# Kernel optimization log

Measured on AMD Instinct MI355X. Metric: run time of the kernel, lower is better.

## Reference

```python
import jax, jax.numpy as jnp
import numpy as np

N = 100000
E = 1600000
IN_C, HID_C, OUT_C, NUM_CLASSES = 128, 64, 64, 40


def glorot(key, shape):
    lim = float(np.sqrt(6.0 / (shape[0] + shape[1])))
    return jax.random.uniform(key, shape, jnp.float32, -lim, lim)


def setup_inputs() -> dict:
    key = jax.random.key(0)
    ks = jax.random.split(key, 8)
    x = jax.random.normal(ks[0], (N, IN_C), jnp.float32)
    edge_index = jax.random.randint(ks[1], (2, E), 0, N, jnp.int64)
    return {
        "x": x,
        "edge_index": edge_index,
        "W1": glorot(ks[2], (IN_C, HID_C)),
        "b1": jnp.zeros((HID_C,), jnp.float32),
        "W2": glorot(ks[3], (HID_C, OUT_C)),
        "b2": jnp.zeros((OUT_C,), jnp.float32),
        "Wf": glorot(ks[4], (OUT_C, NUM_CLASSES)),
        "bf": jnp.zeros((NUM_CLASSES,), jnp.float32),
    }


def gcn_conv(x, W, b, src, dst, n):
    # PyG GCNConv: out = D^{-1/2} (A + I) D^{-1/2} (x W) + b, self-loops added.
    h = x @ W  # [N, C_out]
    loop = jnp.arange(n, dtype=src.dtype)
    src_f = jnp.concatenate([src, loop])  # [E+N]
    dst_f = jnp.concatenate([dst, loop])
    deg = jax.ops.segment_sum(jnp.ones_like(dst_f, dtype=h.dtype), dst_f,
                              num_segments=n)  # in-degree incl. self-loop
    inv_sqrt = jnp.where(deg > 0, jax.lax.rsqrt(deg), 0.0)
    norm = inv_sqrt[src_f] * inv_sqrt[dst_f]  # [E+N]
    msg = h[src_f] * norm[:, None]  # gather + scale, [E+N, C_out]
    out = jax.ops.segment_sum(msg, dst_f, num_segments=n)  # scatter-add
    return out + b


def reference(x, edge_index, W1, b1, W2, b2, Wf, bf):
    src, dst = edge_index[0], edge_index[1]
    n = x.shape[0]
    h = jax.nn.relu(gcn_conv(x, W1, b1, src, dst, n))
    h = jax.nn.relu(gcn_conv(h, W2, b2, src, dst, n))
    return h @ Wf + bf
```

## Files before the change

### kernel.cpp

```cpp
#include <hip/hip_runtime.h>

constexpr int N_NODES = 100000;
constexpr int N_EDGES = 1600000;
constexpr int IN_C  = 128;
constexpr int HID_C = 64;
constexpr int NUM_CLASSES = 40;

constexpr int BSH = 9;
constexpr int BUCK_N = 1 << BSH;
constexpr int NBUCK = (N_NODES + BUCK_N - 1) >> BSH;
constexpr int BCAP = 9216;
constexpr int FS_EPT = 16;
constexpr int FS_T = 256;
constexpr int FS_CHUNK = FS_EPT * FS_T;
constexpr int FS_BLKS = (N_EDGES + FS_CHUNK - 1) / FS_CHUNK;

typedef __attribute__((ext_vector_type(8))) short bf16x8;
typedef __attribute__((ext_vector_type(4))) short short4v;
typedef __attribute__((ext_vector_type(4))) float f32x4;

__device__ __forceinline__ unsigned short f2bf(float f) {
    unsigned u = __float_as_uint(f);
    return (unsigned short)((u + 0x7FFFu + ((u >> 16) & 1u)) >> 16);
}
__device__ __forceinline__ float bf2f(unsigned short h) {
    return __uint_as_float((unsigned)h << 16);
}

__global__ void bucket_init_kernel(unsigned* __restrict__ gcur) {
    if (threadIdx.x < NBUCK) gcur[threadIdx.x] = 0u;
}

__global__ __launch_bounds__(FS_T) void fill_stage_kernel(
        const int* __restrict__ src, const int* __restrict__ dst,
        unsigned* __restrict__ gcur, unsigned* __restrict__ stage) {
    __shared__ unsigned hist[NBUCK];
    __shared__ unsigned rbase[NBUCK];
    int t = threadIdx.x;
    for (int i = t; i < NBUCK; i += FS_T) hist[i] = 0u;
    __syncthreads();
    int e0 = blockIdx.x * FS_CHUNK + t;
    unsigned pay[FS_EPT];
    unsigned br[FS_EPT];
#pragma unroll
    for (int i = 0; i < FS_EPT; ++i) {
        int e = e0 + i * FS_T;
        br[i] = 0xFFFFFFFFu; pay[i] = 0u;
        if (e < N_EDGES) {
            unsigned d = (unsigned)dst[e];
            unsigned s = (unsigned)src[e];
            unsigned b = d >> BSH;
            unsigned r = atomicAdd(&hist[b], 1u);
            pay[i] = (s << BSH) | (d & (BUCK_N - 1u));
            br[i]  = (b << 16) | r;
        }
    }
    __syncthreads();
    for (int i = t; i < NBUCK; i += FS_T) {
        unsigned c = hist[i];
        rbase[i] = c ? ((unsigned)i * BCAP + atomicAdd(&gcur[i], c)) : 0u;
    }
    __syncthreads();
#pragma unroll
    for (int i = 0; i < FS_EPT; ++i) {
        if (br[i] != 0xFFFFFFFFu) {
            unsigned bb = br[i] >> 16;
            unsigned idx = rbase[bb] + (br[i] & 0xFFFFu);
            if (idx < (bb + 1u) * BCAP) stage[idx] = pay[i];
        }
    }
}

__global__ __launch_bounds__(256) void scan_buckets_kernel(
        const unsigned* __restrict__ gcur, unsigned* __restrict__ bbase,
        unsigned* __restrict__ rowptr) {
    __shared__ unsigned s[256];
    int t = threadIdx.x;
    unsigned v = (t < NBUCK) ? gcur[t] : 0u;
    s[t] = v;
    __syncthreads();
    for (int off = 1; off < 256; off <<= 1) {
        unsigned u = (t >= off) ? s[t - off] : 0u;
        __syncthreads();
        s[t] += u;
        __syncthreads();
    }
    if (t < NBUCK) bbase[t] = s[t] - v;
    if (t == 255) rowptr[N_NODES] = s[255];
}

__global__ __launch_bounds__(512) void fill_final_kernel(
        const unsigned* __restrict__ gcur, const unsigned* __restrict__ bbase,
        const unsigned* __restrict__ stage, unsigned* __restrict__ rowptr,
        float* __restrict__ inv, unsigned* __restrict__ csr_src) {
    __shared__ unsigned cur[BUCK_N];
    __shared__ unsigned ps[512];
    __shared__ unsigned buf[BCAP];
    int b = blockIdx.x, t = threadIdx.x;
    int lo = b << BSH;
    int nn = min(BUCK_N, N_NODES - lo);
    unsigned c = min(gcur[b], (unsigned)BCAP);
    unsigned base = bbase[b];
    const unsigned* st = stage + (size_t)b * BCAP;
    cur[t] = 0u;
    __syncthreads();
    for (int i = t; i < (int)c; i += 512) atomicAdd(&cur[st[i] & (BUCK_N - 1u)], 1u);
    __syncthreads();
    unsigned d = cur[t];
    ps[t] = d;
    __syncthreads();
    for (int off = 1; off < 512; off <<= 1) {
        unsigned u = (t >= off) ? ps[t - off] : 0u;
        __syncthreads();
        ps[t] += u;
        __syncthreads();
    }
    unsigned off0 = ps[t] - d;
    if (t < nn) {
        rowptr[lo + t] = base + off0;
        inv[lo + t] = rsqrtf((float)(d + 1u));
    }
    __syncthreads();
    cur[t] = off0;
    __syncthreads();
    for (int i = t; i < (int)c; i += 512) {
        unsigned v = st[i];
        unsigned pos = atomicAdd(&cur[v & (BUCK_N - 1u)], 1u);
        buf[pos] = v >> BSH;
    }
    __syncthreads();
    for (int i = t; i < (int)c; i += 512) csr_src[base + i] = buf[i];
}

template <int K, bool BF>
__global__ __launch_bounds__(256) void gemm_mfma_kernel(
        const void* __restrict__ Xv, const float* __restrict__ W,
        const float* __restrict__ inv, unsigned short* __restrict__ out, int n) {
    __shared__ __align__(16) short Asd[64][K + 8];
    __shared__ __align__(16) short Bsd[64][K + 8];
    int t = threadIdx.x;
    int n0 = blockIdx.x * 64;
    if (BF) {
        const uint4* Xb = (const uint4*)Xv;
        for (int i = t; i < 64 * (K / 8); i += 256) {
            int row = i / (K / 8), seg = i % (K / 8);
            int node = n0 + row;
            uint4 v = {0, 0, 0, 0};
            if (node < n) v = Xb[(size_t)node * (K / 8) + seg];
            *(uint4*)&Asd[row][seg * 8] = v;
        }
    } else {
        const float* Xf = (const float*)Xv;
        for (int i = t; i < 64 * (K / 4); i += 256) {
            int row = i / (K / 4), seg = i % (K / 4);
            int node = n0 + row;
            float4 v = {0, 0, 0, 0};
            if (node < n) v = *(const float4*)&Xf[(size_t)node * K + seg * 4];
            short4v o;
            o.x = (short)f2bf(v.x); o.y = (short)f2bf(v.y);
            o.z = (short)f2bf(v.z); o.w = (short)f2bf(v.w);
            *(short4v*)&Asd[row][seg * 4] = o;
        }
    }
    for (int i = t; i < K * 16; i += 256) {
        int k = i >> 4, ng = i & 15;
        float4 v = *(const float4*)&W[(size_t)k * 64 + ng * 4];
        Bsd[ng * 4 + 0][k] = (short)f2bf(v.x);
        Bsd[ng * 4 + 1][k] = (short)f2bf(v.y);
        Bsd[ng * 4 + 2][k] = (short)f2bf(v.z);
        Bsd[ng * 4 + 3][k] = (short)f2bf(v.w);
    }
    __syncthreads();
    int wv = t >> 6, lane = t & 63;
    int m = lane & 15, quad = lane >> 4;
    int rowbase = wv * 16;
    f32x4 acc0 = {0,0,0,0}, acc1 = {0,0,0,0}, acc2 = {0,0,0,0}, acc3 = {0,0,0,0};
#pragma unroll
    for (int kb = 0; kb < K / 32; ++kb) {
        bf16x8 af = *(const bf16x8*)&Asd[rowbase + m][kb * 32 + quad * 8];
        bf16x8 b0 = *(const bf16x8*)&Bsd[ 0 + m][kb * 32 + quad * 8];
        bf16x8 b1 = *(const bf16x8*)&Bsd[16 + m][kb * 32 + quad * 8];
        bf16x8 b2 = *(const bf16x8*)&Bsd[32 + m][kb * 32 + quad * 8];
        bf16x8 b3 = *(const bf16x8*)&Bsd[48 + m][kb * 32 + quad * 8];
        acc0 = __builtin_amdgcn_mfma_f32_16x16x32_bf16(af, b0, acc0, 0, 0, 0);
        acc1 = __builtin_amdgcn_mfma_f32_16x16x32_bf16(af, b1, acc1, 0, 0, 0);
        acc2 = __builtin_amdgcn_mfma_f32_16x16x32_bf16(af, b2, acc2, 0, 0, 0);
        acc3 = __builtin_amdgcn_mfma_f32_16x16x32_bf16(af, b3, acc3, 0, 0, 0);
    }
    f32x4 accs[4] = {acc0, acc1, acc2, acc3};
#pragma unroll
    for (int r = 0; r < 4; ++r) {
        int node = n0 + rowbase + quad * 4 + r;
        if (node < n) {
            float sc = inv[node];
#pragma unroll
            for (int s = 0; s < 4; ++s)
                out[(size_t)node * 64 + s * 16 + m] = f2bf(accs[s][r] * sc);
        }
    }
}

__global__ __launch_bounds__(256) void agg_fused_kernel(
        const unsigned* __restrict__ rowptr, const unsigned* __restrict__ csr_src,
        const unsigned short* __restrict__ hs, const float* __restrict__ inv,
        const float* __restrict__ bias, unsigned short* __restrict__ out) {
    int node = blockIdx.x * 4 + (threadIdx.x >> 6);
    int lane = threadIdx.x & 63;
    int oct = lane >> 3;
    int cl  = lane & 7;
    unsigned beg = rowptr[node], end = rowptr[node + 1];
    float a0 = 0.f, a1 = 0.f, a2 = 0.f, a3 = 0.f;
    float a4 = 0.f, a5 = 0.f, a6 = 0.f, a7 = 0.f;
    const uint4* hsrow = (const uint4*)hs;
    for (unsigned base = beg; base < end; base += 64) {
        int navail = min((int)(end - base), 64);
        unsigned myidx = 0;
        if (lane < navail) myidx = csr_src[base + lane];
        int it8 = (navail + 7) & ~7;
        for (int i = oct; i < it8; i += 8) {
            unsigned s = __shfl(myidx, i);
            if (i < navail) {
                uint4 v = hsrow[(size_t)s * 8 + cl];
                a0 += __uint_as_float(v.x << 16);
                a1 += __uint_as_float(v.x & 0xFFFF0000u);
                a2 += __uint_as_float(v.y << 16);
                a3 += __uint_as_float(v.y & 0xFFFF0000u);
                a4 += __uint_as_float(v.z << 16);
                a5 += __uint_as_float(v.z & 0xFFFF0000u);
                a6 += __uint_as_float(v.w << 16);
                a7 += __uint_as_float(v.w & 0xFFFF0000u);
            }
        }
    }
    a0 += __shfl_xor(a0, 8);  a1 += __shfl_xor(a1, 8);
    a2 += __shfl_xor(a2, 8);  a3 += __shfl_xor(a3, 8);
    a4 += __shfl_xor(a4, 8);  a5 += __shfl_xor(a5, 8);
    a6 += __shfl_xor(a6, 8);  a7 += __shfl_xor(a7, 8);
    a0 += __shfl_xor(a0, 16); a1 += __shfl_xor(a1, 16);
    a2 += __shfl_xor(a2, 16); a3 += __shfl_xor(a3, 16);
    a4 += __shfl_xor(a4, 16); a5 += __shfl_xor(a5, 16);
    a6 += __shfl_xor(a6, 16); a7 += __shfl_xor(a7, 16);
    a0 += __shfl_xor(a0, 32); a1 += __shfl_xor(a1, 32);
    a2 += __shfl_xor(a2, 32); a3 += __shfl_xor(a3, 32);
    a4 += __shfl_xor(a4, 32); a5 += __shfl_xor(a5, 32);
    a6 += __shfl_xor(a6, 32); a7 += __shfl_xor(a7, 32);
    if (oct == 0) {
        uint4 sv = hsrow[(size_t)node * 8 + cl];
        float4 bv0 = *(const float4*)&bias[cl * 8];
        float4 bv1 = *(const float4*)&bias[cl * 8 + 4];
        float s = inv[node];
        float r0 = fmaxf(s * (a0 + __uint_as_float(sv.x << 16))        + bv0.x, 0.f);
        float r1 = fmaxf(s * (a1 + __uint_as_float(sv.x & 0xFFFF0000u)) + bv0.y, 0.f);
        float r2 = fmaxf(s * (a2 + __uint_as_float(sv.y << 16))        + bv0.z, 0.f);
        float r3 = fmaxf(s * (a3 + __uint_as_float(sv.y & 0xFFFF0000u)) + bv0.w, 0.f);
        float r4 = fmaxf(s * (a4 + __uint_as_float(sv.z << 16))        + bv1.x, 0.f);
        float r5 = fmaxf(s * (a5 + __uint_as_float(sv.z & 0xFFFF0000u)) + bv1.y, 0.f);
        float r6 = fmaxf(s * (a6 + __uint_as_float(sv.w << 16))        + bv1.z, 0.f);
        float r7 = fmaxf(s * (a7 + __uint_as_float(sv.w & 0xFFFF0000u)) + bv1.w, 0.f);
        uint4 o;
        o.x = (unsigned)f2bf(r0) | ((unsigned)f2bf(r1) << 16);
        o.y = (unsigned)f2bf(r2) | ((unsigned)f2bf(r3) << 16);
        o.z = (unsigned)f2bf(r4) | ((unsigned)f2bf(r5) << 16);
        o.w = (unsigned)f2bf(r6) | ((unsigned)f2bf(r7) << 16);
        ((uint4*)out)[(size_t)node * 8 + cl] = o;
    }
}

__global__ __launch_bounds__(320) void final_gemm_kernel(
        const unsigned short* __restrict__ H, const float* __restrict__ Wf,
        const float* __restrict__ bfv, float* __restrict__ out, int n) {
    constexpr int CK = 64, J = 40;
    __shared__ float Ws[CK * J];
    __shared__ float Hs[CK][132];
    int t = threadIdx.x;
    int n0 = blockIdx.x * 128;
    for (int i = t; i < CK * J / 4; i += 320)
        ((float4*)Ws)[i] = ((const float4*)Wf)[i];
    for (int i = t; i < 128 * 16; i += 320) {
        int row = i >> 4, kc = i & 15;
        int node = n0 + row;
        ushort4 v = {0, 0, 0, 0};
        if (node < n) v = *(const ushort4*)&H[(size_t)node * 64 + kc * 4];
        Hs[kc * 4 + 0][row] = bf2f(v.x);
        Hs[kc * 4 + 1][row] = bf2f(v.y);
        Hs[kc * 4 + 2][row] = bf2f(v.z);
        Hs[kc * 4 + 3][row] = bf2f(v.w);
    }
    __syncthreads();
    int cg = t % 10;
    int rg = t / 10;
    float4 a0 = {0,0,0,0}, a1 = {0,0,0,0}, a2 = {0,0,0,0}, a3 = {0,0,0,0};
#pragma unroll 8
    for (int k = 0; k < CK; ++k) {
        float4 b = *(const float4*)&Ws[k * J + cg * 4];
        float4 a = *(const float4*)&Hs[k][rg * 4];
        a0.x += a.x * b.x; a0.y += a.x * b.y; a0.z += a.x * b.z; a0.w += a.x * b.w;
        a1.x += a.y * b.x; a1.y += a.y * b.y; a1.z += a.y * b.z; a1.w += a.y * b.w;
        a2.x += a.z * b.x; a2.y += a.z * b.y; a2.z += a.z * b.z; a2.w += a.z * b.w;
        a3.x += a.w * b.x; a3.y += a.w * b.y; a3.z += a.w * b.z; a3.w += a.w * b.w;
    }
    float4 bv = *(const float4*)&bfv[cg * 4];
    float4 accs[4] = {a0, a1, a2, a3};
#pragma unroll
    for (int i = 0; i < 4; ++i) {
        int node = n0 + rg * 4 + i;
        if (node < n) {
            float4 r = accs[i];
            r.x += bv.x; r.y += bv.y; r.z += bv.z; r.w += bv.w;
            *(float4*)&out[(size_t)node * J + cg * 4] = r;
        }
    }
}

extern "C" void kernel_launch(void* const* d_in, const int* in_sizes, int n_in,
                              void* d_out, int out_size, void* d_ws, size_t ws_size,
                              hipStream_t stream) {
    const float* x  = (const float*)d_in[0];
    const int*   ei = (const int*)d_in[1];
    const float* W1 = (const float*)d_in[2];
    const float* b1 = (const float*)d_in[3];
    const float* W2 = (const float*)d_in[4];
    const float* b2 = (const float*)d_in[5];
    const float* Wf = (const float*)d_in[6];
    const float* bf = (const float*)d_in[7];
    float* out = (float*)d_out;

    const int* src = ei;
    const int* dst = ei + N_EDGES;

    char* ws = (char*)d_ws;
    unsigned* rowptr  = (unsigned*)(ws + 0);
    float*    inv     = (float*)   (ws + 400064);
    unsigned* gcur    = (unsigned*)(ws + 800064);
    unsigned* bbase   = (unsigned*)(ws + 800896);
    unsigned* csr_src = (unsigned*)(ws + 801792);
    unsigned short* A = (unsigned short*)(ws + 7201792);
    unsigned short* B = (unsigned short*)(ws + 20001792);
    unsigned* stage   = (unsigned*)A;

    bucket_init_kernel<<<1, 256, 0, stream>>>(gcur);
    fill_stage_kernel<<<FS_BLKS, FS_T, 0, stream>>>(src, dst, gcur, stage);
    scan_buckets_kernel<<<1, 256, 0, stream>>>(gcur, bbase, rowptr);
    fill_final_kernel<<<NBUCK, 512, 0, stream>>>(gcur, bbase, stage, rowptr, inv, csr_src);

    gemm_mfma_kernel<IN_C, false>
        <<<(N_NODES + 63) / 64, 256, 0, stream>>>(x, W1, inv, A, N_NODES);
    agg_fused_kernel<<<N_NODES / 4, 256, 0, stream>>>(rowptr, csr_src, A, inv, b1, B);

    gemm_mfma_kernel<HID_C, true>
        <<<(N_NODES + 63) / 64, 256, 0, stream>>>(B, W2, inv, A, N_NODES);
    agg_fused_kernel<<<N_NODES / 4, 256, 0, stream>>>(rowptr, csr_src, A, inv, b2, B);

    final_gemm_kernel<<<(N_NODES + 127) / 128, 320, 0, stream>>>(B, Wf, bf, out, N_NODES);
}
```

Before: 274.1 us.

## Map one node per 8-lane group in aggregation instead of one node per wave

The aggregation kernel now gives each wavefront 8 nodes, with one 8-lane group per node, so each group walks its own CSR row serially. Before, each wave served one node and split its edges across 8 octets. This removes the cross-octet shuffle reduction and the idle-lane waste on low-degree nodes (average degree is about 16). In exchange, the groups within a wave diverge when node degrees differ, and the per-edge index loads are no longer coalesced across the wave.

```diff
diff --git a/kernel.cpp b/kernel.cpp
--- a/kernel.cpp
+++ b/kernel.cpp
@@ -204,66 +204,46 @@
         const unsigned* __restrict__ rowptr, const unsigned* __restrict__ csr_src,
         const unsigned short* __restrict__ hs, const float* __restrict__ inv,
         const float* __restrict__ bias, unsigned short* __restrict__ out) {
-    int node = blockIdx.x * 4 + (threadIdx.x >> 6);
-    int lane = threadIdx.x & 63;
+    int t = threadIdx.x;
+    int lane = t & 63;
     int oct = lane >> 3;
     int cl  = lane & 7;
+    int node = blockIdx.x * 32 + (t >> 6) * 8 + oct;
     unsigned beg = rowptr[node], end = rowptr[node + 1];
     float a0 = 0.f, a1 = 0.f, a2 = 0.f, a3 = 0.f;
     float a4 = 0.f, a5 = 0.f, a6 = 0.f, a7 = 0.f;
     const uint4* hsrow = (const uint4*)hs;
-    for (unsigned base = beg; base < end; base += 64) {
-        int navail = min((int)(end - base), 64);
-        unsigned myidx = 0;
-        if (lane < navail) myidx = csr_src[base + lane];
-        int it8 = (navail + 7) & ~7;
-        for (int i = oct; i < it8; i += 8) {
-            unsigned s = __shfl(myidx, i);
-            if (i < navail) {
-                uint4 v = hsrow[(size_t)s * 8 + cl];
-                a0 += __uint_as_float(v.x << 16);
-                a1 += __uint_as_float(v.x & 0xFFFF0000u);
-                a2 += __uint_as_float(v.y << 16);
-                a3 += __uint_as_float(v.y & 0xFFFF0000u);
-                a4 += __uint_as_float(v.z << 16);
-                a5 += __uint_as_float(v.z & 0xFFFF0000u);
-                a6 += __uint_as_float(v.w << 16);
-                a7 += __uint_as_float(v.w & 0xFFFF0000u);
-            }
-        }
-    }
-    a0 += __shfl_xor(a0, 8);  a1 += __shfl_xor(a1, 8);
-    a2 += __shfl_xor(a2, 8);  a3 += __shfl_xor(a3, 8);
-    a4 += __shfl_xor(a4, 8);  a5 += __shfl_xor(a5, 8);
-    a6 += __shfl_xor(a6, 8);  a7 += __shfl_xor(a7, 8);
-    a0 += __shfl_xor(a0, 16); a1 += __shfl_xor(a1, 16);
-    a2 += __shfl_xor(a2, 16); a3 += __shfl_xor(a3, 16);
-    a4 += __shfl_xor(a4, 16); a5 += __shfl_xor(a5, 16);
-    a6 += __shfl_xor(a6, 16); a7 += __shfl_xor(a7, 16);
-    a0 += __shfl_xor(a0, 32); a1 += __shfl_xor(a1, 32);
-    a2 += __shfl_xor(a2, 32); a3 += __shfl_xor(a3, 32);
-    a4 += __shfl_xor(a4, 32); a5 += __shfl_xor(a5, 32);
-    a6 += __shfl_xor(a6, 32); a7 += __shfl_xor(a7, 32);
-    if (oct == 0) {
-        uint4 sv = hsrow[(size_t)node * 8 + cl];
-        float4 bv0 = *(const float4*)&bias[cl * 8];
-        float4 bv1 = *(const float4*)&bias[cl * 8 + 4];
-        float s = inv[node];
-        float r0 = fmaxf(s * (a0 + __uint_as_float(sv.x << 16))        + bv0.x, 0.f);
-        float r1 = fmaxf(s * (a1 + __uint_as_float(sv.x & 0xFFFF0000u)) + bv0.y, 0.f);
-        float r2 = fmaxf(s * (a2 + __uint_as_float(sv.y << 16))        + bv0.z, 0.f);
-        float r3 = fmaxf(s * (a3 + __uint_as_float(sv.y & 0xFFFF0000u)) + bv0.w, 0.f);
-        float r4 = fmaxf(s * (a4 + __uint_as_float(sv.z << 16))        + bv1.x, 0.f);
-        float r5 = fmaxf(s * (a5 + __uint_as_float(sv.z & 0xFFFF0000u)) + bv1.y, 0.f);
-        float r6 = fmaxf(s * (a6 + __uint_as_float(sv.w << 16))        + bv1.z, 0.f);
-        float r7 = fmaxf(s * (a7 + __uint_as_float(sv.w & 0xFFFF0000u)) + bv1.w, 0.f);
-        uint4 o;
-        o.x = (unsigned)f2bf(r0) | ((unsigned)f2bf(r1) << 16);
-        o.y = (unsigned)f2bf(r2) | ((unsigned)f2bf(r3) << 16);
-        o.z = (unsigned)f2bf(r4) | ((unsigned)f2bf(r5) << 16);
-        o.w = (unsigned)f2bf(r6) | ((unsigned)f2bf(r7) << 16);
-        ((uint4*)out)[(size_t)node * 8 + cl] = o;
-    }
+#pragma unroll 4
+    for (unsigned e = beg; e < end; ++e) {
+        unsigned s = csr_src[e];
+        uint4 v = hsrow[(size_t)s * 8 + cl];
+        a0 += __uint_as_float(v.x << 16);
+        a1 += __uint_as_float(v.x & 0xFFFF0000u);
+        a2 += __uint_as_float(v.y << 16);
+        a3 += __uint_as_float(v.y & 0xFFFF0000u);
+        a4 += __uint_as_float(v.z << 16);
+        a5 += __uint_as_float(v.z & 0xFFFF0000u);
+        a6 += __uint_as_float(v.w << 16);
+        a7 += __uint_as_float(v.w & 0xFFFF0000u);
+    }
+    uint4 sv = hsrow[(size_t)node * 8 + cl];
+    float4 bv0 = *(const float4*)&bias[cl * 8];
+    float4 bv1 = *(const float4*)&bias[cl * 8 + 4];
+    float s = inv[node];
+    float r0 = fmaxf(s * (a0 + __uint_as_float(sv.x << 16))         + bv0.x, 0.f);
+    float r1 = fmaxf(s * (a1 + __uint_as_float(sv.x & 0xFFFF0000u)) + bv0.y, 0.f);
+    float r2 = fmaxf(s * (a2 + __uint_as_float(sv.y << 16))         + bv0.z, 0.f);
+    float r3 = fmaxf(s * (a3 + __uint_as_float(sv.y & 0xFFFF0000u)) + bv0.w, 0.f);
+    float r4 = fmaxf(s * (a4 + __uint_as_float(sv.z << 16))         + bv1.x, 0.f);
+    float r5 = fmaxf(s * (a5 + __uint_as_float(sv.z & 0xFFFF0000u)) + bv1.y, 0.f);
+    float r6 = fmaxf(s * (a6 + __uint_as_float(sv.w << 16))         + bv1.z, 0.f);
+    float r7 = fmaxf(s * (a7 + __uint_as_float(sv.w & 0xFFFF0000u)) + bv1.w, 0.f);
+    uint4 o;
+    o.x = (unsigned)f2bf(r0) | ((unsigned)f2bf(r1) << 16);
+    o.y = (unsigned)f2bf(r2) | ((unsigned)f2bf(r3) << 16);
+    o.z = (unsigned)f2bf(r4) | ((unsigned)f2bf(r5) << 16);
+    o.w = (unsigned)f2bf(r6) | ((unsigned)f2bf(r7) << 16);
+    ((uint4*)out)[(size_t)node * 8 + cl] = o;
 }
 
 __global__ __launch_bounds__(320) void final_gemm_kernel(
@@ -345,11 +325,11 @@
 
     gemm_mfma_kernel<IN_C, false>
         <<<(N_NODES + 63) / 64, 256, 0, stream>>>(x, W1, inv, A, N_NODES);
-    agg_fused_kernel<<<N_NODES / 4, 256, 0, stream>>>(rowptr, csr_src, A, inv, b1, B);
+    agg_fused_kernel<<<N_NODES / 32, 256, 0, stream>>>(rowptr, csr_src, A, inv, b1, B);
 
     gemm_mfma_kernel<HID_C, true>
         <<<(N_NODES + 63) / 64, 256, 0, stream>>>(B, W2, inv, A, N_NODES);
-    agg_fused_kernel<<<N_NODES / 4, 256, 0, stream>>>(rowptr, csr_src, A, inv, b2, B);
+    agg_fused_kernel<<<N_NODES / 32, 256, 0, stream>>>(rowptr, csr_src, A, inv, b2, B);
 
     final_gemm_kernel<<<(N_NODES + 127) / 128, 320, 0, stream>>>(B, Wf, bf, out, N_NODES);
 }
```

Result: faster. 244.6 us (-10.8%).
